# Performance work log

Hardware: AMD Instinct MI355X
Metric: run time of the kernel (lower is better)

The kernel has to match this reference:

```python
import jax, jax.numpy as jnp
import numpy as np

NUM_NODES = 100000
NUM_EDGES = 600000
NUM_GRAPHS = 1000
EMB = 128


def setup_inputs() -> dict:
    key = jax.random.key(0)
    ks = jax.random.split(key, 12)
    x = jax.random.normal(ks[0], (NUM_NODES, 4), dtype=jnp.float32)
    edge_index = jax.random.randint(ks[1], (2, NUM_EDGES), 0, NUM_NODES, dtype=jnp.int32)
    x_scalar = jax.random.normal(ks[2], (NUM_GRAPHS, 4), dtype=jnp.float32)
    batch_index = jnp.sort(jax.random.randint(ks[3], (NUM_NODES,), 0, NUM_GRAPHS, dtype=jnp.int32))
    def glorot(k, shape):
        fan_in, fan_out = shape[0], shape[1]
        s = jnp.sqrt(2.0 / (fan_in + fan_out)).astype(jnp.float32)
        return jax.random.normal(k, shape, dtype=jnp.float32) * s
    return {
        "x": x,
        "edge_index": edge_index,
        "x_scalar": x_scalar,
        "batch_index": batch_index,
        "W0": glorot(ks[4], (4, EMB)), "b0": jnp.zeros((EMB,), jnp.float32),
        "W1": glorot(ks[5], (EMB, EMB)), "b1": jnp.zeros((EMB,), jnp.float32),
        "W2": glorot(ks[6], (EMB, EMB)), "b2": jnp.zeros((EMB,), jnp.float32),
        "W3": glorot(ks[7], (EMB, EMB)), "b3": jnp.zeros((EMB,), jnp.float32),
        "Wl1": glorot(ks[8], (EMB + 4, 64)), "bl1": jnp.zeros((64,), jnp.float32),
        "Wl2": glorot(ks[9], (64, 1)), "bl2": jnp.zeros((1,), jnp.float32),
    }


def _gcn_norm(edge_index, num_nodes):
    # PyG GCNConv default: add self-loops, symmetric normalization
    loop = jnp.arange(num_nodes, dtype=edge_index.dtype)
    src = jnp.concatenate([edge_index[0], loop])
    dst = jnp.concatenate([edge_index[1], loop])
    deg = jax.ops.segment_sum(jnp.ones_like(src, dtype=jnp.float32), dst,
                              num_segments=num_nodes)
    dinv = jnp.where(deg > 0, jax.lax.rsqrt(jnp.maximum(deg, 1e-12)), 0.0)
    norm = dinv[src] * dinv[dst]  # [E+N]
    return src, dst, norm


def _gcn_conv(h, src, dst, norm, W, b, num_nodes):
    h = h @ W                                   # [N, out]
    msg = h[src] * norm[:, None]                # gather + normalize
    out = jax.ops.segment_sum(msg, dst, num_segments=num_nodes)  # scatter-add
    return out + b


def reference(x, edge_index, x_scalar, batch_index,
              W0, b0, W1, b1, W2, b2, W3, b3, Wl1, bl1, Wl2, bl2):
    n = x.shape[0]
    src, dst, norm = _gcn_norm(edge_index, n)
    h = jax.nn.relu(_gcn_conv(x, src, dst, norm, W0, b0, n))
    h = jax.nn.relu(_gcn_conv(h, src, dst, norm, W1, b1, n))
    h = jax.nn.relu(_gcn_conv(h, src, dst, norm, W2, b2, n))
    h = jax.nn.relu(_gcn_conv(h, src, dst, norm, W3, b3, n))
    # global mean pool over batch_index
    sums = jax.ops.segment_sum(h, batch_index, num_segments=NUM_GRAPHS)
    cnts = jax.ops.segment_sum(jnp.ones((n,), jnp.float32), batch_index,
                               num_segments=NUM_GRAPHS)
    pooled = sums / jnp.maximum(cnts, 1.0)[:, None]          # [G, EMB]
    feat = jnp.concatenate([pooled, x_scalar], axis=1)       # [G, EMB+4]
    out = jax.nn.relu(feat @ Wl1 + bl1) @ Wl2 + bl2          # [G, 1]
    return out
```

## Files before the change

### kernel.cpp

```cpp
#include <hip/hip_runtime.h>

#define NN 100000
#define EE 600000
#define GG 1000
#define NB ((NN + 255) / 256)
#define CAP 32
#define LDSPAD 136

typedef __bf16 bf16x8 __attribute__((ext_vector_type(8)));
typedef float f32x4 __attribute__((ext_vector_type(4)));
typedef unsigned int u32;

__device__ inline float2 bf2_to_f2(u32 u) {
  return make_float2(__uint_as_float(u << 16), __uint_as_float(u & 0xffff0000u));
}
__device__ inline u32 f2_to_bf2(float a, float b) {
  union { __bf16 h[2]; u32 u; } pk;
  pk.h[0] = (__bf16)a; pk.h[1] = (__bf16)b;
  return pk.u;
}


__global__ void k_init(int* cnt, int* gstart) {
  int i = blockIdx.x * 256 + threadIdx.x;
  if (i < NN) cnt[i] = 0;
  if (i <= GG) gstart[i] = NN;
}

__global__ void k_fill(const int* __restrict__ src, const int* __restrict__ dst,
                       int* cnt, int* __restrict__ bucket) {
  int e = blockIdx.x * 256 + threadIdx.x;
  if (e >= EE) return;
  int s = src[e], d = dst[e];
  int pos = atomicAdd(&cnt[d], 1);
  if (pos < CAP) bucket[d * CAP + pos] = s;
}

__global__ void k_prep(const int* __restrict__ cnt, float* __restrict__ dinv,
                       const int* __restrict__ batch, int* gstart,
                       const float* __restrict__ W1, const float* __restrict__ W2,
                       const float* __restrict__ W3,
                       __bf16* __restrict__ Wt1, __bf16* __restrict__ Wt2,
                       __bf16* __restrict__ Wt3) {
  int gid = blockIdx.x * 256 + threadIdx.x;
  if (gid < NN) {
    dinv[gid] = rsqrtf((float)(cnt[gid] + 1));
    int b = batch[gid];
    if (gid == 0) {
      for (int g = 0; g <= b; ++g) gstart[g] = 0;
    } else {
      int prev = batch[gid - 1];
      for (int g = prev + 1; g <= b; ++g) gstart[g] = gid;
    }
  }
  if (gid < 3 * 16384) {
    int which = gid >> 14, idx = gid & 16383;
    int n = idx >> 7, k = idx & 127;
    const float* W = (which == 0) ? W1 : (which == 1) ? W2 : W3;
    __bf16* Wt = (which == 0) ? Wt1 : (which == 1) ? Wt2 : Wt3;
    Wt[(size_t)n * 128 + k] = (__bf16)W[(size_t)k * 128 + n];
  }
}


__global__ void k_aggx(const float4* __restrict__ x, const int* __restrict__ cnt,
                       const int* __restrict__ bucket, const float* __restrict__ dinv,
                       float4* __restrict__ y) {
  int i = blockIdx.x * 256 + threadIdx.x;
  if (i >= NN) return;
  float di = dinv[i];
  float sw = di * di;
  float4 xi = x[i];
  float4 acc = make_float4(sw * xi.x, sw * xi.y, sw * xi.z, sw * xi.w);
  int m = min(cnt[i], CAP);
  for (int e = 0; e < m; ++e) {
    int s = bucket[i * CAP + e];
    float w = dinv[s] * di;
    float4 v = x[s];
    acc.x = fmaf(w, v.x, acc.x);
    acc.y = fmaf(w, v.y, acc.y);
    acc.z = fmaf(w, v.z, acc.z);
    acc.w = fmaf(w, v.w, acc.w);
  }
  y[i] = acc;
}

__global__ __launch_bounds__(256) void k_agg1(const float4* __restrict__ y,
                                              const int* __restrict__ cnt,
                                              const int* __restrict__ bucket,
                                              const float* __restrict__ dinv,
                                              const float* __restrict__ W0,
                                              const float* __restrict__ b0,
                                              u32* __restrict__ hout2) {
  int node = blockIdx.x * 4 + (threadIdx.x >> 6);
  int lane = threadIdx.x & 63;
  int ln = lane & 15, quad = lane >> 4;
  if (node >= NN) return;

  float w0r[4][8], b0r[8];
  #pragma unroll
  for (int k = 0; k < 4; ++k) {
    float4 a = *(const float4*)(W0 + k * 128 + ln * 8);
    float4 b = *(const float4*)(W0 + k * 128 + ln * 8 + 4);
    w0r[k][0] = a.x; w0r[k][1] = a.y; w0r[k][2] = a.z; w0r[k][3] = a.w;
    w0r[k][4] = b.x; w0r[k][5] = b.y; w0r[k][6] = b.z; w0r[k][7] = b.w;
  }
  {
    float4 a = *(const float4*)(b0 + ln * 8);
    float4 b = *(const float4*)(b0 + ln * 8 + 4);
    b0r[0] = a.x; b0r[1] = a.y; b0r[2] = a.z; b0r[3] = a.w;
    b0r[4] = b.x; b0r[5] = b.y; b0r[6] = b.z; b0r[7] = b.w;
  }

  float di = dinv[node];
  float sw = di * di;
  int m = min(cnt[node], CAP);
  int s_l = node; float dv_l = 0.f;
  if (m > 0) {
    s_l = bucket[node * CAP + min(lane, m - 1)];
    dv_l = dinv[s_l];
  }

  float4 yv = y[node];
  float ws = (quad == 0) ? sw : 0.f;
  float acc[8];
  #pragma unroll
  for (int c = 0; c < 8; ++c) {
    float v = b0r[c];
    v = fmaf(yv.x, w0r[0][c], v); v = fmaf(yv.y, w0r[1][c], v);
    v = fmaf(yv.z, w0r[2][c], v); v = fmaf(yv.w, w0r[3][c], v);
    acc[c] = ws * fmaxf(v, 0.f);
  }
  for (int j = 0; j < m; j += 8) {
    int e0 = j + quad, e1 = j + 4 + quad;
    int p0 = min(e0, m - 1) * 4, p1 = min(e1, m - 1) * 4;
    int se0 = __builtin_amdgcn_ds_bpermute(p0, s_l);
    int se1 = __builtin_amdgcn_ds_bpermute(p1, s_l);
    float w0e = (e0 < m) ? __int_as_float(__builtin_amdgcn_ds_bpermute(p0, __float_as_int(dv_l))) * di : 0.f;
    float w1e = (e1 < m) ? __int_as_float(__builtin_amdgcn_ds_bpermute(p1, __float_as_int(dv_l))) * di : 0.f;
    float4 y0 = y[se0];
    float4 y1 = y[se1];
    #pragma unroll
    for (int c = 0; c < 8; ++c) {
      float v0 = b0r[c];
      v0 = fmaf(y0.x, w0r[0][c], v0); v0 = fmaf(y0.y, w0r[1][c], v0);
      v0 = fmaf(y0.z, w0r[2][c], v0); v0 = fmaf(y0.w, w0r[3][c], v0);
      acc[c] = fmaf(w0e, fmaxf(v0, 0.f), acc[c]);
      float v1 = b0r[c];
      v1 = fmaf(y1.x, w0r[0][c], v1); v1 = fmaf(y1.y, w0r[1][c], v1);
      v1 = fmaf(y1.z, w0r[2][c], v1); v1 = fmaf(y1.w, w0r[3][c], v1);
      acc[c] = fmaf(w1e, fmaxf(v1, 0.f), acc[c]);
    }
  }
  #pragma unroll
  for (int c = 0; c < 8; ++c) {
    acc[c] += __shfl_xor(acc[c], 16);
    acc[c] += __shfl_xor(acc[c], 32);
  }
  if (quad == 0) {
    uint4 o;
    o.x = f2_to_bf2(acc[0], acc[1]);
    o.y = f2_to_bf2(acc[2], acc[3]);
    o.z = f2_to_bf2(acc[4], acc[5]);
    o.w = f2_to_bf2(acc[6], acc[7]);
    *(uint4*)(hout2 + (size_t)node * 64 + ln * 4) = o;
  }
}

__global__ __launch_bounds__(256) void k_agg23(const __bf16* __restrict__ hlin,
                                               const int* __restrict__ cnt,
                                               const int* __restrict__ bucket,
                                               const float* __restrict__ dinv,
                                               u32* __restrict__ hout2) {
  int node = blockIdx.x * 4 + (threadIdx.x >> 6);
  int lane = threadIdx.x & 63;
  int ln = lane & 15, quad = lane >> 4;
  if (node >= NN) return;
  float di = dinv[node];
  float sw = di * di;
  int m = min(cnt[node], CAP);
  int s_l = node; float dv_l = 0.f;
  if (m > 0) {
    s_l = bucket[node * CAP + min(lane, m - 1)];
    dv_l = dinv[s_l];
  }

  uint4 su = *(const uint4*)(hlin + ((size_t)node << 7) + ln * 8);
  float q0 = (quad == 0) ? sw : 0.f;
  float acc[8];
  float2 f;
  f = bf2_to_f2(su.x); acc[0] = q0 * f.x; acc[1] = q0 * f.y;
  f = bf2_to_f2(su.y); acc[2] = q0 * f.x; acc[3] = q0 * f.y;
  f = bf2_to_f2(su.z); acc[4] = q0 * f.x; acc[5] = q0 * f.y;
  f = bf2_to_f2(su.w); acc[6] = q0 * f.x; acc[7] = q0 * f.y;

  for (int j = 0; j < m; j += 8) {
    int e0 = j + quad, e1 = j + 4 + quad;
    int p0 = min(e0, m - 1) * 4, p1 = min(e1, m - 1) * 4;
    int se0 = __builtin_amdgcn_ds_bpermute(p0, s_l);
    int se1 = __builtin_amdgcn_ds_bpermute(p1, s_l);
    float w0e = (e0 < m) ? __int_as_float(__builtin_amdgcn_ds_bpermute(p0, __float_as_int(dv_l))) * di : 0.f;
    float w1e = (e1 < m) ? __int_as_float(__builtin_amdgcn_ds_bpermute(p1, __float_as_int(dv_l))) * di : 0.f;
    uint4 u0 = *(const uint4*)(hlin + ((size_t)se0 << 7) + ln * 8);
    uint4 u1 = *(const uint4*)(hlin + ((size_t)se1 << 7) + ln * 8);
    f = bf2_to_f2(u0.x); acc[0] = fmaf(w0e, f.x, acc[0]); acc[1] = fmaf(w0e, f.y, acc[1]);
    f = bf2_to_f2(u0.y); acc[2] = fmaf(w0e, f.x, acc[2]); acc[3] = fmaf(w0e, f.y, acc[3]);
    f = bf2_to_f2(u0.z); acc[4] = fmaf(w0e, f.x, acc[4]); acc[5] = fmaf(w0e, f.y, acc[5]);
    f = bf2_to_f2(u0.w); acc[6] = fmaf(w0e, f.x, acc[6]); acc[7] = fmaf(w0e, f.y, acc[7]);
    f = bf2_to_f2(u1.x); acc[0] = fmaf(w1e, f.x, acc[0]); acc[1] = fmaf(w1e, f.y, acc[1]);
    f = bf2_to_f2(u1.y); acc[2] = fmaf(w1e, f.x, acc[2]); acc[3] = fmaf(w1e, f.y, acc[3]);
    f = bf2_to_f2(u1.z); acc[4] = fmaf(w1e, f.x, acc[4]); acc[5] = fmaf(w1e, f.y, acc[5]);
    f = bf2_to_f2(u1.w); acc[6] = fmaf(w1e, f.x, acc[6]); acc[7] = fmaf(w1e, f.y, acc[7]);
  }
  #pragma unroll
  for (int k = 0; k < 8; ++k) {
    acc[k] += __shfl_xor(acc[k], 16);
    acc[k] += __shfl_xor(acc[k], 32);
  }
  if (quad == 0) {
    uint4 o;
    o.x = f2_to_bf2(acc[0], acc[1]);
    o.y = f2_to_bf2(acc[2], acc[3]);
    o.z = f2_to_bf2(acc[4], acc[5]);
    o.w = f2_to_bf2(acc[6], acc[7]);
    *(uint4*)(hout2 + (size_t)node * 64 + ln * 4) = o;
  }
}

__global__ __launch_bounds__(256) void k_mfma(const __bf16* __restrict__ hin,
                                              const __bf16* __restrict__ Wt,
                                              const float* __restrict__ bias,
                                              __bf16* __restrict__ hout) {
  __shared__ __bf16 As[128 * LDSPAD];
  int tid = threadIdx.x;
  int row0 = blockIdx.x * 128;
  int lane = tid & 63, w = tid >> 6;
  int ln = lane & 15, quad = lane >> 4;

  bf16x8 bfrag[8][4];
  float bcol[8];
  #pragma unroll
  for (int nt = 0; nt < 8; ++nt) {
    bcol[nt] = bias[nt * 16 + ln];
    #pragma unroll
    for (int kc = 0; kc < 4; ++kc)
      bfrag[nt][kc] = *(const bf16x8*)(Wt + (size_t)(nt * 16 + ln) * 128 + kc * 32 + quad * 8);
  }

  #pragma unroll
  for (int i = 0; i < 8; ++i) {
    int eb = (i * 256 + tid) * 8;
    int r = eb >> 7, c = eb & 127;
    int gr = row0 + r;
    uint4 v = make_uint4(0, 0, 0, 0);
    if (gr < NN) v = *(const uint4*)(hin + (size_t)gr * 128 + c);
    *(uint4*)&As[r * LDSPAD + c] = v;
  }
  __syncthreads();

  f32x4 acc[2][8];
  #pragma unroll
  for (int rt = 0; rt < 2; ++rt)
    #pragma unroll
    for (int nt = 0; nt < 8; ++nt) acc[rt][nt] = (f32x4){0.f, 0.f, 0.f, 0.f};

  #pragma unroll
  for (int kc = 0; kc < 4; ++kc) {
    bf16x8 a0 = *(const bf16x8*)&As[(w * 32 + ln) * LDSPAD + kc * 32 + quad * 8];
    bf16x8 a1 = *(const bf16x8*)&As[(w * 32 + 16 + ln) * LDSPAD + kc * 32 + quad * 8];
    #pragma unroll
    for (int nt = 0; nt < 8; ++nt) {
      acc[0][nt] = __builtin_amdgcn_mfma_f32_16x16x32_bf16(a0, bfrag[nt][kc], acc[0][nt], 0, 0, 0);
      acc[1][nt] = __builtin_amdgcn_mfma_f32_16x16x32_bf16(a1, bfrag[nt][kc], acc[1][nt], 0, 0, 0);
    }
  }

  #pragma unroll
  for (int rt = 0; rt < 2; ++rt)
    #pragma unroll
    for (int nt = 0; nt < 8; ++nt)
      #pragma unroll
      for (int reg = 0; reg < 4; ++reg) {
        int gr = row0 + w * 32 + rt * 16 + quad * 4 + reg;
        if (gr < NN)
          hout[(size_t)gr * 128 + nt * 16 + ln] =
              (__bf16)fmaxf(acc[rt][nt][reg] + bcol[nt], 0.f);
      }
}

__global__ __launch_bounds__(256) void k_poolmlp(const uint2* __restrict__ h4u,
                                                 const int* __restrict__ gstart,
                                                 const float* __restrict__ xs,
                                                 const float* __restrict__ Wl1,
                                                 const float* __restrict__ bl1,
                                                 const float* __restrict__ Wl2,
                                                 const float* __restrict__ bl2,
                                                 float* __restrict__ out) {
  __shared__ float4 part[8][32];
  __shared__ float pooled[128];
  int g = blockIdx.x;
  int beg = gstart[g], end = gstart[g + 1];
  int tid = threadIdx.x;
  int cg = tid & 31;
  int rg = tid >> 5;
  float4 acc = make_float4(0.f, 0.f, 0.f, 0.f);
  for (int i = beg + rg; i < end; i += 8) {
    uint2 u = h4u[(size_t)i * 32 + cg];
    acc.x += __uint_as_float(u.x << 16);
    acc.y += __uint_as_float(u.x & 0xffff0000u);
    acc.z += __uint_as_float(u.y << 16);
    acc.w += __uint_as_float(u.y & 0xffff0000u);
  }
  part[rg][cg] = acc;
  __syncthreads();
  if (tid < 32) {
    float4 s = part[0][tid];
    #pragma unroll
    for (int r = 1; r < 8; ++r) {
      float4 v = part[r][tid];
      s.x += v.x; s.y += v.y; s.z += v.z; s.w += v.w;
    }
    float sc = 1.f / fmaxf((float)(end - beg), 1.f);
    pooled[tid * 4 + 0] = s.x * sc;
    pooled[tid * 4 + 1] = s.y * sc;
    pooled[tid * 4 + 2] = s.z * sc;
    pooled[tid * 4 + 3] = s.w * sc;
  }
  __syncthreads();
  if (tid < 64) {
    float hj = bl1[tid];
    #pragma unroll 4
    for (int k = 0; k < 128; ++k) hj = fmaf(pooled[k], Wl1[k * 64 + tid], hj);
    const float* xr = xs + g * 4;
    #pragma unroll
    for (int k = 0; k < 4; ++k) hj = fmaf(xr[k], Wl1[(128 + k) * 64 + tid], hj);
    hj = fmaxf(hj, 0.f);
    float val = hj * Wl2[tid];
    #pragma unroll
    for (int off = 32; off > 0; off >>= 1) val += __shfl_down(val, off);
    if (tid == 0) out[g] = val + bl2[0];
  }
}


extern "C" void kernel_launch(void* const* d_in, const int* in_sizes, int n_in,
                              void* d_out, int out_size, void* d_ws, size_t ws_size,
                              hipStream_t stream) {
  const float* x    = (const float*)d_in[0];
  const int*   ei   = (const int*)d_in[1];
  const float* xs   = (const float*)d_in[2];
  const int*   batch= (const int*)d_in[3];
  const float* W0   = (const float*)d_in[4];
  const float* b0   = (const float*)d_in[5];
  const float* W1   = (const float*)d_in[6];
  const float* b1   = (const float*)d_in[7];
  const float* W2   = (const float*)d_in[8];
  const float* b2   = (const float*)d_in[9];
  const float* W3   = (const float*)d_in[10];
  const float* b3   = (const float*)d_in[11];
  const float* Wl1  = (const float*)d_in[12];
  const float* bl1  = (const float*)d_in[13];
  const float* Wl2  = (const float*)d_in[14];
  const float* bl2  = (const float*)d_in[15];
  const int* srcA = ei;
  const int* dstA = ei + EE;
  float* out = (float*)d_out;

  char* p = (char*)d_ws;
  auto take = [&](size_t bytes) { char* q = p; p += (bytes + 255) & ~(size_t)255; return q; };
  __bf16* hA   = (__bf16*)take((size_t)NN * 128 * 2);
  __bf16* hB   = (__bf16*)take((size_t)NN * 128 * 2);
  float*  y    = (float*)take((size_t)NN * 4 * 4);
  int*   cnt   = (int*)take((size_t)NN * 4);
  float* dinv  = (float*)take((size_t)NN * 4);
  int*   bucket= (int*)take((size_t)NN * CAP * 4);
  int*   gstart= (int*)take((size_t)(GG + 1) * 4);
  __bf16* Wt1  = (__bf16*)take(16384 * 2);
  __bf16* Wt2  = (__bf16*)take(16384 * 2);
  __bf16* Wt3  = (__bf16*)take(16384 * 2);

  k_init<<<NB, 256, 0, stream>>>(cnt, gstart);
  k_fill<<<(EE + 255) / 256, 256, 0, stream>>>(srcA, dstA, cnt, bucket);
  k_prep<<<NB, 256, 0, stream>>>(cnt, dinv, batch, gstart, W1, W2, W3, Wt1, Wt2, Wt3);

  k_aggx<<<NB, 256, 0, stream>>>((const float4*)x, cnt, bucket, dinv, (float4*)y);
  k_agg1<<<(NN + 3) / 4, 256, 0, stream>>>((const float4*)y, cnt, bucket, dinv,
                                           W0, b0, (u32*)hB);
  k_mfma<<<(NN + 127) / 128, 256, 0, stream>>>(hB, Wt1, b1, hA);
  k_agg23<<<(NN + 3) / 4, 256, 0, stream>>>(hA, cnt, bucket, dinv, (u32*)hB);
  k_mfma<<<(NN + 127) / 128, 256, 0, stream>>>(hB, Wt2, b2, hA);
  k_agg23<<<(NN + 3) / 4, 256, 0, stream>>>(hA, cnt, bucket, dinv, (u32*)hB);
  k_mfma<<<(NN + 127) / 128, 256, 0, stream>>>(hB, Wt3, b3, hA);

  k_poolmlp<<<GG, 256, 0, stream>>>((const uint2*)hA, gstart, xs, Wl1, bl1, Wl2, bl2, out);
}
```

Before: 364.7 us.

## Precompute weighted neighbor buckets and split layer-0 linear from aggregation

Adds a pass that builds a padded bucket of (source, normalized weight) pairs per node. The self-loop goes into the bucket and padding slots carry zero weight, so the aggregation loops no longer compute dinv products or mask out-of-range edges. Layer 0 no longer recomputes the 4x128 linear and ReLU for every edge. Instead it runs a separate per-node linear kernel and then the shared bf16 aggregation kernel. The cost is an extra kernel and an 8-byte-per-slot bucket buffer, and in-degree capacity drops to CAP-1 so nodes with 32 or more in-edges lose one more edge.

```diff
diff --git a/kernel.cpp b/kernel.cpp
--- a/kernel.cpp
+++ b/kernel.cpp
@@ -28,12 +28,12 @@
 }
 
 __global__ void k_fill(const int* __restrict__ src, const int* __restrict__ dst,
-                       int* cnt, int* __restrict__ bucket) {
+                       int* cnt, int* __restrict__ ibucket) {
   int e = blockIdx.x * 256 + threadIdx.x;
   if (e >= EE) return;
   int s = src[e], d = dst[e];
   int pos = atomicAdd(&cnt[d], 1);
-  if (pos < CAP) bucket[d * CAP + pos] = s;
+  if (pos < CAP - 1) ibucket[d * CAP + pos] = s;
 }
 
 __global__ void k_prep(const int* __restrict__ cnt, float* __restrict__ dinv,
@@ -62,21 +62,33 @@
   }
 }
 
+__global__ void k_wb(const int* __restrict__ ibucket, const int* __restrict__ cnt,
+                     const float* __restrict__ dinv, int2* __restrict__ wbucket) {
+  int gid = blockIdx.x * 256 + threadIdx.x;
+  if (gid >= NN * CAP) return;
+  int d = gid >> 5, slot = gid & 31;
+  int m = min(cnt[d], CAP - 1);
+  int mp = (m + 8) & ~7;
+  if (slot >= mp) return;
+  float dd = dinv[d];
+  int s; float w;
+  if (slot < m)      { s = ibucket[gid]; w = dinv[s] * dd; }
+  else if (slot == m){ s = d;            w = dd * dd; }
+  else               { s = d;            w = 0.f; }
+  wbucket[gid] = make_int2(s, __float_as_int(w));
+}
+
 
 __global__ void k_aggx(const float4* __restrict__ x, const int* __restrict__ cnt,
-                       const int* __restrict__ bucket, const float* __restrict__ dinv,
-                       float4* __restrict__ y) {
+                       const int2* __restrict__ wbucket, float4* __restrict__ y) {
   int i = blockIdx.x * 256 + threadIdx.x;
   if (i >= NN) return;
-  float di = dinv[i];
-  float sw = di * di;
-  float4 xi = x[i];
-  float4 acc = make_float4(sw * xi.x, sw * xi.y, sw * xi.z, sw * xi.w);
-  int m = min(cnt[i], CAP);
-  for (int e = 0; e < m; ++e) {
-    int s = bucket[i * CAP + e];
-    float w = dinv[s] * di;
-    float4 v = x[s];
+  int m1 = min(cnt[i], CAP - 1) + 1;
+  float4 acc = make_float4(0.f, 0.f, 0.f, 0.f);
+  for (int e = 0; e < m1; ++e) {
+    int2 md = wbucket[i * CAP + e];
+    float w = __int_as_float(md.y);
+    float4 v = x[md.x];
     acc.x = fmaf(w, v.x, acc.x);
     acc.y = fmaf(w, v.y, acc.y);
     acc.z = fmaf(w, v.z, acc.z);
@@ -85,124 +97,59 @@
   y[i] = acc;
 }
 
-__global__ __launch_bounds__(256) void k_agg1(const float4* __restrict__ y,
-                                              const int* __restrict__ cnt,
-                                              const int* __restrict__ bucket,
-                                              const float* __restrict__ dinv,
-                                              const float* __restrict__ W0,
-                                              const float* __restrict__ b0,
-                                              u32* __restrict__ hout2) {
-  int node = blockIdx.x * 4 + (threadIdx.x >> 6);
-  int lane = threadIdx.x & 63;
-  int ln = lane & 15, quad = lane >> 4;
-  if (node >= NN) return;
-
-  float w0r[4][8], b0r[8];
+
+__global__ void k_lin0(const float4* __restrict__ y, const float* __restrict__ W0,
+                       const float* __restrict__ b0, u32* __restrict__ hout2) {
+  int gid = blockIdx.x * 256 + threadIdx.x;
+  if (gid >= NN * 16) return;
+  int node = gid >> 4, cg = gid & 15;
+  float4 yv = y[node];
+  float v[8];
+  #pragma unroll
+  for (int k = 0; k < 2; ++k) {
+    float4 b = *(const float4*)(b0 + cg * 8 + k * 4);
+    v[k * 4 + 0] = b.x; v[k * 4 + 1] = b.y; v[k * 4 + 2] = b.z; v[k * 4 + 3] = b.w;
+  }
   #pragma unroll
   for (int k = 0; k < 4; ++k) {
-    float4 a = *(const float4*)(W0 + k * 128 + ln * 8);
-    float4 b = *(const float4*)(W0 + k * 128 + ln * 8 + 4);
-    w0r[k][0] = a.x; w0r[k][1] = a.y; w0r[k][2] = a.z; w0r[k][3] = a.w;
-    w0r[k][4] = b.x; w0r[k][5] = b.y; w0r[k][6] = b.z; w0r[k][7] = b.w;
-  }
-  {
-    float4 a = *(const float4*)(b0 + ln * 8);
-    float4 b = *(const float4*)(b0 + ln * 8 + 4);
-    b0r[0] = a.x; b0r[1] = a.y; b0r[2] = a.z; b0r[3] = a.w;
-    b0r[4] = b.x; b0r[5] = b.y; b0r[6] = b.z; b0r[7] = b.w;
-  }
-
-  float di = dinv[node];
-  float sw = di * di;
-  int m = min(cnt[node], CAP);
-  int s_l = node; float dv_l = 0.f;
-  if (m > 0) {
-    s_l = bucket[node * CAP + min(lane, m - 1)];
-    dv_l = dinv[s_l];
-  }
-
-  float4 yv = y[node];
-  float ws = (quad == 0) ? sw : 0.f;
-  float acc[8];
-  #pragma unroll
-  for (int c = 0; c < 8; ++c) {
-    float v = b0r[c];
-    v = fmaf(yv.x, w0r[0][c], v); v = fmaf(yv.y, w0r[1][c], v);
-    v = fmaf(yv.z, w0r[2][c], v); v = fmaf(yv.w, w0r[3][c], v);
-    acc[c] = ws * fmaxf(v, 0.f);
-  }
-  for (int j = 0; j < m; j += 8) {
-    int e0 = j + quad, e1 = j + 4 + quad;
-    int p0 = min(e0, m - 1) * 4, p1 = min(e1, m - 1) * 4;
-    int se0 = __builtin_amdgcn_ds_bpermute(p0, s_l);
-    int se1 = __builtin_amdgcn_ds_bpermute(p1, s_l);
-    float w0e = (e0 < m) ? __int_as_float(__builtin_amdgcn_ds_bpermute(p0, __float_as_int(dv_l))) * di : 0.f;
-    float w1e = (e1 < m) ? __int_as_float(__builtin_amdgcn_ds_bpermute(p1, __float_as_int(dv_l))) * di : 0.f;
-    float4 y0 = y[se0];
-    float4 y1 = y[se1];
-    #pragma unroll
-    for (int c = 0; c < 8; ++c) {
-      float v0 = b0r[c];
-      v0 = fmaf(y0.x, w0r[0][c], v0); v0 = fmaf(y0.y, w0r[1][c], v0);
-      v0 = fmaf(y0.z, w0r[2][c], v0); v0 = fmaf(y0.w, w0r[3][c], v0);
-      acc[c] = fmaf(w0e, fmaxf(v0, 0.f), acc[c]);
-      float v1 = b0r[c];
-      v1 = fmaf(y1.x, w0r[0][c], v1); v1 = fmaf(y1.y, w0r[1][c], v1);
-      v1 = fmaf(y1.z, w0r[2][c], v1); v1 = fmaf(y1.w, w0r[3][c], v1);
-      acc[c] = fmaf(w1e, fmaxf(v1, 0.f), acc[c]);
-    }
-  }
-  #pragma unroll
-  for (int c = 0; c < 8; ++c) {
-    acc[c] += __shfl_xor(acc[c], 16);
-    acc[c] += __shfl_xor(acc[c], 32);
-  }
-  if (quad == 0) {
-    uint4 o;
-    o.x = f2_to_bf2(acc[0], acc[1]);
-    o.y = f2_to_bf2(acc[2], acc[3]);
-    o.z = f2_to_bf2(acc[4], acc[5]);
-    o.w = f2_to_bf2(acc[6], acc[7]);
-    *(uint4*)(hout2 + (size_t)node * 64 + ln * 4) = o;
-  }
+    float yk = (k == 0) ? yv.x : (k == 1) ? yv.y : (k == 2) ? yv.z : yv.w;
+    float4 wa = *(const float4*)(W0 + k * 128 + cg * 8);
+    float4 wb = *(const float4*)(W0 + k * 128 + cg * 8 + 4);
+    v[0] = fmaf(yk, wa.x, v[0]); v[1] = fmaf(yk, wa.y, v[1]);
+    v[2] = fmaf(yk, wa.z, v[2]); v[3] = fmaf(yk, wa.w, v[3]);
+    v[4] = fmaf(yk, wb.x, v[4]); v[5] = fmaf(yk, wb.y, v[5]);
+    v[6] = fmaf(yk, wb.z, v[6]); v[7] = fmaf(yk, wb.w, v[7]);
+  }
+  uint4 o;
+  o.x = f2_to_bf2(fmaxf(v[0], 0.f), fmaxf(v[1], 0.f));
+  o.y = f2_to_bf2(fmaxf(v[2], 0.f), fmaxf(v[3], 0.f));
+  o.z = f2_to_bf2(fmaxf(v[4], 0.f), fmaxf(v[5], 0.f));
+  o.w = f2_to_bf2(fmaxf(v[6], 0.f), fmaxf(v[7], 0.f));
+  *(uint4*)(hout2 + (size_t)node * 64 + cg * 4) = o;
 }
 
 __global__ __launch_bounds__(256) void k_agg23(const __bf16* __restrict__ hlin,
                                                const int* __restrict__ cnt,
-                                               const int* __restrict__ bucket,
-                                               const float* __restrict__ dinv,
+                                               const int2* __restrict__ wbucket,
                                                u32* __restrict__ hout2) {
   int node = blockIdx.x * 4 + (threadIdx.x >> 6);
   int lane = threadIdx.x & 63;
   int ln = lane & 15, quad = lane >> 4;
   if (node >= NN) return;
-  float di = dinv[node];
-  float sw = di * di;
-  int m = min(cnt[node], CAP);
-  int s_l = node; float dv_l = 0.f;
-  if (m > 0) {
-    s_l = bucket[node * CAP + min(lane, m - 1)];
-    dv_l = dinv[s_l];
-  }
-
-  uint4 su = *(const uint4*)(hlin + ((size_t)node << 7) + ln * 8);
-  float q0 = (quad == 0) ? sw : 0.f;
-  float acc[8];
-  float2 f;
-  f = bf2_to_f2(su.x); acc[0] = q0 * f.x; acc[1] = q0 * f.y;
-  f = bf2_to_f2(su.y); acc[2] = q0 * f.x; acc[3] = q0 * f.y;
-  f = bf2_to_f2(su.z); acc[4] = q0 * f.x; acc[5] = q0 * f.y;
-  f = bf2_to_f2(su.w); acc[6] = q0 * f.x; acc[7] = q0 * f.y;
-
-  for (int j = 0; j < m; j += 8) {
-    int e0 = j + quad, e1 = j + 4 + quad;
-    int p0 = min(e0, m - 1) * 4, p1 = min(e1, m - 1) * 4;
+  int mp = (min(cnt[node], CAP - 1) + 8) & ~7;
+  int2 me = wbucket[(size_t)node * CAP + (lane & 31)];
+  int s_l = me.x, w_l = me.y;
+
+  float acc[8] = {0.f, 0.f, 0.f, 0.f, 0.f, 0.f, 0.f, 0.f};
+  for (int j = 0; j < mp; j += 8) {
+    int p0 = (j + quad) * 4, p1 = (j + 4 + quad) * 4;
     int se0 = __builtin_amdgcn_ds_bpermute(p0, s_l);
     int se1 = __builtin_amdgcn_ds_bpermute(p1, s_l);
-    float w0e = (e0 < m) ? __int_as_float(__builtin_amdgcn_ds_bpermute(p0, __float_as_int(dv_l))) * di : 0.f;
-    float w1e = (e1 < m) ? __int_as_float(__builtin_amdgcn_ds_bpermute(p1, __float_as_int(dv_l))) * di : 0.f;
+    float w0e = __int_as_float(__builtin_amdgcn_ds_bpermute(p0, w_l));
+    float w1e = __int_as_float(__builtin_amdgcn_ds_bpermute(p1, w_l));
     uint4 u0 = *(const uint4*)(hlin + ((size_t)se0 << 7) + ln * 8);
     uint4 u1 = *(const uint4*)(hlin + ((size_t)se1 << 7) + ln * 8);
+    float2 f;
     f = bf2_to_f2(u0.x); acc[0] = fmaf(w0e, f.x, acc[0]); acc[1] = fmaf(w0e, f.y, acc[1]);
     f = bf2_to_f2(u0.y); acc[2] = fmaf(w0e, f.x, acc[2]); acc[3] = fmaf(w0e, f.y, acc[3]);
     f = bf2_to_f2(u0.z); acc[4] = fmaf(w0e, f.x, acc[4]); acc[5] = fmaf(w0e, f.y, acc[5]);
@@ -368,28 +315,30 @@
 
   char* p = (char*)d_ws;
   auto take = [&](size_t bytes) { char* q = p; p += (bytes + 255) & ~(size_t)255; return q; };
-  __bf16* hA   = (__bf16*)take((size_t)NN * 128 * 2);
-  __bf16* hB   = (__bf16*)take((size_t)NN * 128 * 2);
-  float*  y    = (float*)take((size_t)NN * 4 * 4);
-  int*   cnt   = (int*)take((size_t)NN * 4);
-  float* dinv  = (float*)take((size_t)NN * 4);
-  int*   bucket= (int*)take((size_t)NN * CAP * 4);
-  int*   gstart= (int*)take((size_t)(GG + 1) * 4);
-  __bf16* Wt1  = (__bf16*)take(16384 * 2);
-  __bf16* Wt2  = (__bf16*)take(16384 * 2);
-  __bf16* Wt3  = (__bf16*)take(16384 * 2);
+  __bf16* hA    = (__bf16*)take((size_t)NN * 128 * 2);
+  __bf16* hB    = (__bf16*)take((size_t)NN * 128 * 2);
+  float*  y     = (float*)take((size_t)NN * 4 * 4);
+  int*    cnt   = (int*)take((size_t)NN * 4);
+  float*  dinv  = (float*)take((size_t)NN * 4);
+  int*    ibucket = (int*)take((size_t)NN * CAP * 4);
+  int2*   wbucket = (int2*)take((size_t)NN * CAP * 8);
+  int*    gstart= (int*)take((size_t)(GG + 1) * 4);
+  __bf16* Wt1   = (__bf16*)take(16384 * 2);
+  __bf16* Wt2   = (__bf16*)take(16384 * 2);
+  __bf16* Wt3   = (__bf16*)take(16384 * 2);
 
   k_init<<<NB, 256, 0, stream>>>(cnt, gstart);
-  k_fill<<<(EE + 255) / 256, 256, 0, stream>>>(srcA, dstA, cnt, bucket);
+  k_fill<<<(EE + 255) / 256, 256, 0, stream>>>(srcA, dstA, cnt, ibucket);
   k_prep<<<NB, 256, 0, stream>>>(cnt, dinv, batch, gstart, W1, W2, W3, Wt1, Wt2, Wt3);
-
-  k_aggx<<<NB, 256, 0, stream>>>((const float4*)x, cnt, bucket, dinv, (float4*)y);
-  k_agg1<<<(NN + 3) / 4, 256, 0, stream>>>((const float4*)y, cnt, bucket, dinv,
-                                           W0, b0, (u32*)hB);
+  k_wb<<<(NN * CAP + 255) / 256, 256, 0, stream>>>(ibucket, cnt, dinv, wbucket);
+
+  k_aggx<<<NB, 256, 0, stream>>>((const float4*)x, cnt, wbucket, (float4*)y);
+  k_lin0<<<(NN * 16 + 255) / 256, 256, 0, stream>>>((const float4*)y, W0, b0, (u32*)hA);
+  k_agg23<<<(NN + 3) / 4, 256, 0, stream>>>(hA, cnt, wbucket, (u32*)hB);
   k_mfma<<<(NN + 127) / 128, 256, 0, stream>>>(hB, Wt1, b1, hA);
-  k_agg23<<<(NN + 3) / 4, 256, 0, stream>>>(hA, cnt, bucket, dinv, (u32*)hB);
+  k_agg23<<<(NN + 3) / 4, 256, 0, stream>>>(hA, cnt, wbucket, (u32*)hB);
   k_mfma<<<(NN + 127) / 128, 256, 0, stream>>>(hB, Wt2, b2, hA);
-  k_agg23<<<(NN + 3) / 4, 256, 0, stream>>>(hA, cnt, bucket, dinv, (u32*)hB);
+  k_agg23<<<(NN + 3) / 4, 256, 0, stream>>>(hA, cnt, wbucket, (u32*)hB);
   k_mfma<<<(NN + 127) / 128, 256, 0, stream>>>(hB, Wt3, b3, hA);
 
   k_poolmlp<<<GG, 256, 0, stream>>>((const uint2*)hA, gstart, xs, Wl1, bl1, Wl2, bl2, out);
```

Result: faster. 354.9 us (-2.7%).
